# Kernel tuning notes

Measured on AMD Instinct MI355X. Metric: run time of the kernel, lower is better.

The kernel has to match this reference:

```python
import jax, jax.numpy as jnp
from jax import lax
import numpy as np

B, N, NPOINT, NSAMPLE, C = 4, 8192, 2048, 32, 128
RADIUS = 0.2
H1, H2, OUT = 64, 128, 128  # mlp: (3+C)->H1->H2, sas: H2->OUT


def fps(xyz, npoint):
    # furthest point sampling: xyz (B,N,3) -> idx (B,npoint) int32
    b, n, _ = xyz.shape
    init_idx = jnp.zeros((b,), jnp.int32)

    def step(carry, _):
        dist, last = carry
        p = jnp.take_along_axis(xyz, last[:, None, None], axis=1)  # (B,1,3)
        d = jnp.sum((xyz - p) ** 2, axis=-1)                       # (B,N)
        dist = jnp.minimum(dist, d)
        nxt = jnp.argmax(dist, axis=-1).astype(jnp.int32)
        return (dist, nxt), nxt

    (_, _), rest = lax.scan(step, (jnp.full((b, n), 1e10, jnp.float32), init_idx),
                            None, length=npoint - 1)
    return jnp.concatenate([init_idx[None, :], rest], axis=0).T    # (B,npoint)


def ball_query(xyz, new_xyz, radius, nsample):
    # xyz (B,N,3), new_xyz (B,S,3) -> idx (B,S,nsample) int32
    n = xyz.shape[1]
    d2 = jnp.sum((new_xyz[:, :, None, :] - xyz[:, None, :, :]) ** 2, axis=-1)  # (B,S,N)
    ar = jnp.arange(n, dtype=jnp.int32)
    keys = jnp.where(d2 <= radius * radius, ar, n)  # valid -> own index, invalid -> N
    neg_vals, _ = lax.top_k(-keys, nsample)          # smallest nsample keys
    idx = -neg_vals
    first = idx[..., :1]
    return jnp.where(idx >= n, first, idx)           # pad invalid with first valid


def gather_points(pts, idx):
    # pts (B,N,D), idx (B,S,ns) -> (B,S,ns,D)
    b, s, ns = idx.shape
    flat = jnp.take_along_axis(pts, idx.reshape(b, s * ns, 1), axis=1)
    return flat.reshape(b, s, ns, -1)


def setup_inputs() -> dict:
    key = jax.random.key(0)
    ks = jax.random.split(key, 8)
    xyz = jax.random.uniform(ks[0], (B, N, 3), dtype=jnp.float32)
    features = jax.random.normal(ks[1], (B, C, N), dtype=jnp.float32)
    cin = C + 3
    W1 = jax.random.normal(ks[2], (H1, cin), dtype=jnp.float32) / np.sqrt(cin)
    b1 = jnp.zeros((H1,), jnp.float32)
    W2 = jax.random.normal(ks[3], (H2, H1), dtype=jnp.float32) / np.sqrt(H1)
    b2 = jnp.zeros((H2,), jnp.float32)
    Wsa = jax.random.normal(ks[4], (OUT, H2), dtype=jnp.float32) / np.sqrt(H2)
    bsa = jnp.zeros((OUT,), jnp.float32)
    return {"xyz": xyz, "features": features, "W1": W1, "b1": b1,
            "W2": W2, "b2": b2, "Wsa": Wsa, "bsa": bsa}


def reference(xyz, features, W1, b1, W2, b2, Wsa, bsa):
    center_idx = fps(xyz, NPOINT)                                   # (B,S)
    new_xyz = jnp.take_along_axis(xyz, center_idx[:, :, None], axis=1)  # (B,S,3)
    g_idx = ball_query(xyz, new_xyz, RADIUS, NSAMPLE)               # (B,S,ns)
    g_xyz = gather_points(xyz, g_idx) - new_xyz[:, :, None, :]      # (B,S,ns,3) relative coords
    g_feat = gather_points(features.transpose(0, 2, 1), g_idx)      # (B,S,ns,C)
    h = jnp.concatenate([g_xyz, g_feat], axis=-1)                   # (B,S,ns,3+C)
    h = jax.nn.relu(jnp.einsum('bsnc,oc->bsno', h, W1) + b1)        # shared 1x1-conv MLP
    h = jax.nn.relu(jnp.einsum('bsnc,oc->bsno', h, W2) + b2)
    pooled = jnp.max(h, axis=2)                                     # max over nsample -> (B,S,H2)
    out = jnp.einsum('bsc,oc->bso', pooled, Wsa) + bsa              # sas channel mixer
    return new_xyz, out.transpose(0, 2, 1)                          # (B,S,3), (B,OUT,S)
```

## Files before the change

kernel.cpp:

```cpp
#include <hip/hip_runtime.h>
#include <cstdint>
#include <cstddef>

#define NB 4
#define NN 8192
#define NPTS 2048
#define NSAMP 32
#define NC 128
#define CIN 131
#define NH1 64
#define NH2 128
#define NOUTC 128
#define GCELLS 4096

typedef float v2f __attribute__((ext_vector_type(2)));

__device__ __forceinline__ float d2_exact(float ax, float ay, float az,
                                          float bx, float by, float bz) {
  float dx = ax - bx, dy = ay - by, dz = az - bz;
  return __fadd_rn(__fadd_rn(__fmul_rn(dx, dx), __fmul_rn(dy, dy)),
                   __fmul_rn(dz, dz));
}

#if __has_builtin(__builtin_amdgcn_mov_dpp)
template <int CTRL>
__device__ __forceinline__ float dppf(float v) {
  return __int_as_float(
      __builtin_amdgcn_mov_dpp(__float_as_int(v), CTRL, 0xF, 0xF, true));
}
template <int CTRL>
__device__ __forceinline__ int dppi(int v) {
  return __builtin_amdgcn_mov_dpp(v, CTRL, 0xF, 0xF, true);
}
#else
template <int CTRL>
__device__ __forceinline__ float dppf(float v) {
  const int m = (CTRL == 0xB1) ? 1 : (CTRL == 0x4E) ? 2 : (CTRL == 0x141) ? 7 : 15;
  return __shfl_xor(v, m);
}
template <int CTRL>
__device__ __forceinline__ int dppi(int v) {
  const int m = (CTRL == 0xB1) ? 1 : (CTRL == 0x4E) ? 2 : (CTRL == 0x141) ? 7 : 15;
  return __shfl_xor(v, m);
}
#endif

__device__ __forceinline__ void red_pair(float& bv, int& bi, float ov, int oi) {
  bool t = (ov > bv) || (ov == bv && oi < bi);
  bv = t ? ov : bv;
  bi = t ? oi : bi;
}
template <int CTRL>
__device__ __forceinline__ void red5(float& v, int& i, float& x, float& y,
                                     float& z) {
  float ov = dppf<CTRL>(v);
  int oi = dppi<CTRL>(i);
  float ox = dppf<CTRL>(x), oy = dppf<CTRL>(y), oz = dppf<CTRL>(z);
  bool t = (ov > v) || (ov == v && oi < i);
  v = t ? ov : v; i = t ? oi : i;
  x = t ? ox : x; y = t ? oy : y; z = t ? oz : z;
}

__device__ __forceinline__ int spread3(int v) {
  return (v & 1) | ((v & 2) << 2) | ((v & 4) << 4) | ((v & 8) << 6);
}

__global__ __launch_bounds__(1024, 1) void sort_kernel(
    const float* __restrict__ xyz, float* __restrict__ xs,
    float* __restrict__ ys, float* __restrict__ zs, int* __restrict__ io) {
  __shared__ int hist[GCELLS];
  __shared__ int cbase[GCELLS];
  __shared__ int wtot[16];
  __shared__ int woff[16];
  const int b = blockIdx.x;
  const int tid = threadIdx.x;
  const int lane = tid & 63;
  const int wid = tid >> 6;
  const float* xb = xyz + (size_t)b * NN * 3;
  for (int i = tid; i < GCELLS; i += 1024) hist[i] = 0;
  __syncthreads();
  int cell[8];
  float px[8], py[8], pz[8];
#pragma unroll
  for (int k = 0; k < 8; ++k) {
    int j = tid + (k << 10);
    float x = xb[j * 3 + 0], y = xb[j * 3 + 1], z = xb[j * 3 + 2];
    px[k] = x; py[k] = y; pz[k] = z;
    int cx = min(15, max(0, (int)(x * 16.0f)));
    int cy = min(15, max(0, (int)(y * 16.0f)));
    int cz = min(15, max(0, (int)(z * 16.0f)));
    cell[k] = spread3(cx) | (spread3(cy) << 1) | (spread3(cz) << 2);
    atomicAdd(&hist[cell[k]], 1);
  }
  __syncthreads();
  const int i0 = tid * 4;
  int h0 = hist[i0], h1 = hist[i0 + 1], h2 = hist[i0 + 2], h3 = hist[i0 + 3];
  int s4 = h0 + h1 + h2 + h3;
  int v = s4;
#pragma unroll
  for (int d = 1; d < 64; d <<= 1) {
    int o = __shfl_up(v, d);
    if (lane >= d) v += o;
  }
  if (lane == 63) wtot[wid] = v;
  __syncthreads();
  if (tid < 16) {
    int acc = 0;
    for (int w = 0; w < 16; ++w) {
      if (w == tid) woff[tid] = acc;
      acc += wtot[w];
    }
  }
  __syncthreads();
  int eb = woff[wid] + v - s4;
  cbase[i0] = eb;
  cbase[i0 + 1] = eb + h0;
  cbase[i0 + 2] = eb + h0 + h1;
  cbase[i0 + 3] = eb + h0 + h1 + h2;
  __syncthreads();
  for (int i = tid; i < GCELLS; i += 1024) hist[i] = 0;
  __syncthreads();
  const size_t bo = (size_t)b * NN;
#pragma unroll
  for (int k = 0; k < 8; ++k) {
    int pos = cbase[cell[k]] + atomicAdd(&hist[cell[k]], 1);
    xs[bo + pos] = px[k];
    ys[bo + pos] = py[k];
    zs[bo + pos] = zs == nullptr ? 0.f : pz[k];
    io[bo + pos] = tid + (k << 10);
  }
}

__global__ __launch_bounds__(1024, 1) void fps_kernel(
    const float* __restrict__ xyz, const float* __restrict__ xs,
    const float* __restrict__ ys, const float* __restrict__ zs,
    const int* __restrict__ io, float* __restrict__ newxyz) {
#pragma clang fp contract(off)
  const int b = blockIdx.x;
  const int tid = threadIdx.x;
  const int lane = tid & 63;
  const int wid = tid >> 6;
  const size_t bo = (size_t)b * NN;

  float X[8], Y[8], Z[8], D[8];
  int I[8];
  float gcx, gcy, gcz, gr;
  {
    float mx = 0.f, my = 0.f, mz = 0.f;
#pragma unroll
    for (int k = 0; k < 8; ++k) {
      int s = tid * 8 + k;
      X[k] = xs[bo + s];
      Y[k] = ys[bo + s];
      Z[k] = zs[bo + s];
      I[k] = io[bo + s];
      D[k] = 1e30f;
      mx += X[k]; my += Y[k]; mz += Z[k];
    }
    mx *= 0.125f; my *= 0.125f; mz *= 0.125f;
    float r2m = 0.f;
#pragma unroll
    for (int k = 0; k < 8; ++k)
      r2m = fmaxf(r2m, d2_exact(X[k], Y[k], Z[k], mx, my, mz));
    gcx = mx; gcy = my; gcz = mz;
    gr = __fmul_rn(sqrtf(r2m), 1.0001f) + 1e-6f;
  }
  float gv = -1.0f;
  int gidx = 0x3fffffff;
  float bwx = 0.f, bwy = 0.f, bwz = 0.f;
  float T = 3e38f;
  float cv = -1.0f; int ci = 0x3fffffff;
  float ccx = 0.f, ccy = 0.f, ccz = 0.f;

  __shared__ float sv[2][16];
  __shared__ int si[2][16];
  __shared__ float sxx[2][16], syy[2][16], szz[2][16];

  const float* xb = xyz + (size_t)b * NN * 3;
  float cx = xb[0], cy = xb[1], cz = xb[2];
  if (tid == 0) {
    newxyz[(size_t)b * NPTS * 3 + 0] = cx;
    newxyz[(size_t)b * NPTS * 3 + 1] = cy;
    newxyz[(size_t)b * NPTS * 3 + 2] = cz;
  }

  for (int t = 1; t < NPTS; ++t) {
    const int par = t & 1;
    const float d2c = d2_exact(gcx, gcy, gcz, cx, cy, cz);
    const bool dirty = d2c < T;
    if (dirty) {
      float nv = -1.0f; int ni = 0x3fffffff;
      float nx = 0.f, ny = 0.f, nz = 0.f;
#pragma unroll
      for (int k = 0; k < 8; ++k) {
        float d2 = d2_exact(X[k], Y[k], Z[k], cx, cy, cz);
        float nd = fminf(D[k], d2);
        D[k] = nd;
        bool c = (nd > nv) || (nd == nv && I[k] < ni);
        nv = c ? nd : nv; ni = c ? I[k] : ni;
        nx = c ? X[k] : nx; ny = c ? Y[k] : ny; nz = c ? Z[k] : nz;
      }
      gv = nv; gidx = ni; bwx = nx; bwy = ny; bwz = nz;
      float s = __fadd_rn(__fmul_rn(sqrtf(nv), 1.0001f), __fadd_rn(gr, 2e-3f));
      T = __fmul_rn(__fmul_rn(s, s), 1.0001f);
    }
    if (__ballot(dirty) != 0ull) {
      float rv = gv; int ri = gidx;
      red_pair(rv, ri, dppf<0xB1>(rv), dppi<0xB1>(ri));
      red_pair(rv, ri, dppf<0x4E>(rv), dppi<0x4E>(ri));
      red_pair(rv, ri, dppf<0x141>(rv), dppi<0x141>(ri));
      red_pair(rv, ri, dppf<0x140>(rv), dppi<0x140>(ri));
      red_pair(rv, ri, __shfl_xor(rv, 16), __shfl_xor(ri, 16));
      red_pair(rv, ri, __shfl_xor(rv, 32), __shfl_xor(ri, 32));
      unsigned long long m = __ballot(gidx == ri);
      int owner = (int)__builtin_ctzll(m);
      cv = rv; ci = ri;
      ccx = __shfl(bwx, owner);
      ccy = __shfl(bwy, owner);
      ccz = __shfl(bwz, owner);
    }
    if (lane == 0) {
      sv[par][wid] = cv; si[par][wid] = ci;
      sxx[par][wid] = ccx; syy[par][wid] = ccy; szz[par][wid] = ccz;
    }
    __syncthreads();
    const int sl = lane & 15;
    float v = sv[par][sl];
    int i = si[par][sl];
    float xx = sxx[par][sl], yy = syy[par][sl], zz = szz[par][sl];
    red5<0xB1>(v, i, xx, yy, zz);
    red5<0x4E>(v, i, xx, yy, zz);
    red5<0x141>(v, i, xx, yy, zz);
    red5<0x140>(v, i, xx, yy, zz);
    cx = xx; cy = yy; cz = zz;
    if (gidx == i) {
      size_t o = ((size_t)b * NPTS + t) * 3;
      newxyz[o + 0] = xx; newxyz[o + 1] = yy; newxyz[o + 2] = zz;
    }
  }
}

__global__ __launch_bounds__(1024, 1) void fps_nosort_kernel(
    const float* __restrict__ xyz, float* __restrict__ newxyz) {
#pragma clang fp contract(off)
  const int b = blockIdx.x;
  const int tid = threadIdx.x;
  const int lane = tid & 63;
  const int wid = tid >> 6;
  const float* xb = xyz + (size_t)b * NN * 3;
  v2f x2[4], y2[4], z2[4], dd[4];
#pragma unroll
  for (int p = 0; p < 4; ++p) {
    int j0 = tid + ((2 * p) << 10);
    int j1 = tid + ((2 * p + 1) << 10);
    x2[p].x = xb[j0 * 3 + 0]; x2[p].y = xb[j1 * 3 + 0];
    y2[p].x = xb[j0 * 3 + 1]; y2[p].y = xb[j1 * 3 + 1];
    z2[p].x = xb[j0 * 3 + 2]; z2[p].y = xb[j1 * 3 + 2];
    dd[p].x = 1e10f; dd[p].y = 1e10f;
  }
  __shared__ float vbuf[2][16];
  __shared__ int ibuf[2][16];
  __shared__ float cbuf[2][16][3];
  float cx = xb[0], cy = xb[1], cz = xb[2];
  if (tid == 0) {
    newxyz[(size_t)b * NPTS * 3 + 0] = cx;
    newxyz[(size_t)b * NPTS * 3 + 1] = cy;
    newxyz[(size_t)b * NPTS * 3 + 2] = cz;
  }
  for (int t = 1; t < NPTS; ++t) {
    const int par = t & 1;
    float bv = -1.0f; int bi = 0;
    float bwx = 0.f, bwy = 0.f, bwz = 0.f;
#pragma unroll
    for (int p = 0; p < 4; ++p) {
      v2f dx = x2[p] - (v2f){cx, cx};
      v2f dy = y2[p] - (v2f){cy, cy};
      v2f dz = z2[p] - (v2f){cz, cz};
      v2f s = dx * dx + dy * dy + dz * dz;
      v2f nd;
      nd.x = fminf(dd[p].x, s.x);
      nd.y = fminf(dd[p].y, s.y);
      dd[p] = nd;
      { bool c = nd.x > bv;
        bv = c ? nd.x : bv; bi = c ? (tid + ((2 * p) << 10)) : bi;
        bwx = c ? x2[p].x : bwx; bwy = c ? y2[p].x : bwy; bwz = c ? z2[p].x : bwz; }
      { bool c = nd.y > bv;
        bv = c ? nd.y : bv; bi = c ? (tid + ((2 * p + 1) << 10)) : bi;
        bwx = c ? x2[p].y : bwx; bwy = c ? y2[p].y : bwy; bwz = c ? z2[p].y : bwz; }
    }
    red_pair(bv, bi, dppf<0xB1>(bv), dppi<0xB1>(bi));
    red_pair(bv, bi, dppf<0x4E>(bv), dppi<0x4E>(bi));
    red_pair(bv, bi, dppf<0x141>(bv), dppi<0x141>(bi));
    red_pair(bv, bi, dppf<0x140>(bv), dppi<0x140>(bi));
    red_pair(bv, bi, __shfl_xor(bv, 16), __shfl_xor(bi, 16));
    red_pair(bv, bi, __shfl_xor(bv, 32), __shfl_xor(bi, 32));
    if (tid == (bi & 1023)) {
      vbuf[par][wid] = bv; ibuf[par][wid] = bi;
      cbuf[par][wid][0] = bwx; cbuf[par][wid][1] = bwy; cbuf[par][wid][2] = bwz;
    }
    __syncthreads();
    float v2w = vbuf[par][lane & 15];
    int i2w = ibuf[par][lane & 15];
    red_pair(v2w, i2w, dppf<0xB1>(v2w), dppi<0xB1>(i2w));
    red_pair(v2w, i2w, dppf<0x4E>(v2w), dppi<0x4E>(i2w));
    red_pair(v2w, i2w, dppf<0x141>(v2w), dppi<0x141>(i2w));
    red_pair(v2w, i2w, dppf<0x140>(v2w), dppi<0x140>(i2w));
    const int slot = (i2w & 1023) >> 6;
    cx = cbuf[par][slot][0]; cy = cbuf[par][slot][1]; cz = cbuf[par][slot][2];
    if (tid == (i2w & 1023)) {
      size_t o = ((size_t)b * NPTS + t) * 3;
      newxyz[o + 0] = cx; newxyz[o + 1] = cy; newxyz[o + 2] = cz;
    }
  }
}

__global__ __launch_bounds__(256) void ballq_kernel(
    const float* __restrict__ xyz, const float* __restrict__ newxyz,
    int* __restrict__ bidx) {
  const int cid = blockIdx.x * 4 + (threadIdx.x >> 6);
  const int lane = threadIdx.x & 63;
  const int b = cid >> 11;
  const float* xb = xyz + (size_t)b * NN * 3;
  const float cx = newxyz[(size_t)cid * 3 + 0];
  const float cy = newxyz[(size_t)cid * 3 + 1];
  const float cz = newxyz[(size_t)cid * 3 + 2];
  int* ob = bidx + (size_t)cid * NSAMP;
  int total = 0;
  int first = -1;
  for (int c0 = 0; c0 < NN; c0 += 64) {
    int j = c0 + lane;
    float xx = xb[j * 3 + 0], yy = xb[j * 3 + 1], zz = xb[j * 3 + 2];
    float d2 = d2_exact(cx, cy, cz, xx, yy, zz);
    bool in = d2 <= 0.04f;
    unsigned long long m = __ballot(in);
    if (first < 0 && m) first = c0 + __builtin_ctzll(m);
    int pos = total + __popcll(m & ((1ull << lane) - 1ull));
    if (in && pos < NSAMP) ob[pos] = j;
    total += __popcll(m);
    if (total >= NSAMP) break;
  }
  if (total < NSAMP && lane < NSAMP - total) ob[total + lane] = first;
}

__global__ void tw_kernel(const float* __restrict__ W1, const float* __restrict__ W2,
                          const float* __restrict__ Wsa, float* __restrict__ w1t,
                          float* __restrict__ w2t, float* __restrict__ wsat) {
  int i = blockIdx.x * blockDim.x + threadIdx.x;
  if (i < CIN * NH1) w1t[i] = W1[(i % NH1) * CIN + (i / NH1)];
  if (i < NH1 * NH2) w2t[i] = W2[(i % NH2) * NH1 + (i / NH2)];
  if (i < NH2 * NOUTC) wsat[i] = Wsa[(i % NOUTC) * NH2 + (i / NOUTC)];
}

__global__ void tfeat_kernel(const float* __restrict__ feat, float* __restrict__ featT) {
  __shared__ float tile[32][33];
  const int b = blockIdx.z;
  const int n0 = blockIdx.x * 32, c0 = blockIdx.y * 32;
  const int tx = threadIdx.x, ty = threadIdx.y;
#pragma unroll
  for (int r = 0; r < 4; ++r)
    tile[ty + r * 8][tx] = feat[((size_t)b * NC + c0 + ty + r * 8) * NN + n0 + tx];
  __syncthreads();
#pragma unroll
  for (int r = 0; r < 4; ++r)
    featT[((size_t)b * NN + n0 + ty + r * 8) * NC + c0 + tx] = tile[tx][ty + r * 8];
}

#define HS 36
__global__ __launch_bounds__(256) void mlp_kernel(
    const float* __restrict__ xyz, const float* __restrict__ fsrc,
    const float* __restrict__ newxyz, const int* __restrict__ bidx,
    const float* __restrict__ w1t, const float* __restrict__ b1,
    const float* __restrict__ w2t, const float* __restrict__ b2,
    const float* __restrict__ wsat, const float* __restrict__ bsa,
    float* __restrict__ out1, int useT) {
  __shared__ float h[CIN * HS];
  __shared__ float h1[NH1 * HS];
  __shared__ float pl[256];
  __shared__ float pooled[NH2];
  __shared__ int sidx[NSAMP];
  __shared__ float sc[3];
  const int cid = blockIdx.x;
  const int b = cid >> 11;
  const int s = cid & 2047;
  const int tid = threadIdx.x;
  if (tid < NSAMP) sidx[tid] = bidx[(size_t)cid * NSAMP + tid];
  if (tid < 3) sc[tid] = newxyz[(size_t)cid * 3 + tid];
  __syncthreads();
  {
    const int ss = tid >> 3, q = tid & 7;
    const int j = sidx[ss];
    if (useT) {
      const float4* fr = (const float4*)(fsrc + ((size_t)b * NN + j) * NC + q * 16);
#pragma unroll
      for (int u = 0; u < 4; ++u) {
        float4 v = fr[u];
        int c = 3 + q * 16 + u * 4;
        h[(c + 0) * HS + ss] = v.x;
        h[(c + 1) * HS + ss] = v.y;
        h[(c + 2) * HS + ss] = v.z;
        h[(c + 3) * HS + ss] = v.w;
      }
    } else {
      for (int u = 0; u < 16; ++u) {
        int c = q * 16 + u;
        h[(3 + c) * HS + ss] = fsrc[((size_t)b * NC + c) * NN + j];
      }
    }
    if (q == 0) {
      const float* pr = xyz + ((size_t)b * NN + j) * 3;
      h[0 * HS + ss] = pr[0] - sc[0];
      h[1 * HS + ss] = pr[1] - sc[1];
      h[2 * HS + ss] = pr[2] - sc[2];
    }
  }
  __syncthreads();
  {
    const int o = tid & 63, sg = tid >> 6;
    float acc[8];
    const float bb = b1[o];
#pragma unroll
    for (int i = 0; i < 8; ++i) acc[i] = bb;
    const float4* hb = (const float4*)&h[sg * 8];
    for (int k = 0; k < CIN; ++k) {
      float w = w1t[k * NH1 + o];
      float4 a = hb[k * (HS / 4) + 0];
      float4 c = hb[k * (HS / 4) + 1];
      acc[0] = fmaf(w, a.x, acc[0]); acc[1] = fmaf(w, a.y, acc[1]);
      acc[2] = fmaf(w, a.z, acc[2]); acc[3] = fmaf(w, a.w, acc[3]);
      acc[4] = fmaf(w, c.x, acc[4]); acc[5] = fmaf(w, c.y, acc[5]);
      acc[6] = fmaf(w, c.z, acc[6]); acc[7] = fmaf(w, c.w, acc[7]);
    }
#pragma unroll
    for (int i = 0; i < 8; ++i) h1[o * HS + sg * 8 + i] = fmaxf(acc[i], 0.0f);
  }
  __syncthreads();
  {
    const int o = tid & 127, sg = tid >> 7;
    float acc[16];
    const float bb = b2[o];
#pragma unroll
    for (int i = 0; i < 16; ++i) acc[i] = bb;
    const float4* hb = (const float4*)&h1[sg * 16];
    for (int k = 0; k < NH1; ++k) {
      float w = w2t[k * NH2 + o];
#pragma unroll
      for (int u = 0; u < 4; ++u) {
        float4 a = hb[k * (HS / 4) + u];
        acc[u * 4 + 0] = fmaf(w, a.x, acc[u * 4 + 0]);
        acc[u * 4 + 1] = fmaf(w, a.y, acc[u * 4 + 1]);
        acc[u * 4 + 2] = fmaf(w, a.z, acc[u * 4 + 2]);
        acc[u * 4 + 3] = fmaf(w, a.w, acc[u * 4 + 3]);
      }
    }
    float pm = acc[0];
#pragma unroll
    for (int i = 1; i < 16; ++i) pm = fmaxf(pm, acc[i]);
    pl[sg * 128 + o] = pm;
  }
  __syncthreads();
  if (tid < NH2) pooled[tid] = fmaxf(fmaxf(pl[tid], pl[128 + tid]), 0.0f);
  __syncthreads();
  if (tid < NOUTC) {
    float acc = bsa[tid];
    for (int k = 0; k < NH2; ++k) acc = fmaf(pooled[k], wsat[k * NOUTC + tid], acc);
    out1[((size_t)b * NOUTC + tid) * NPTS + s] = acc;
  }
}

extern "C" void kernel_launch(void* const* d_in, const int* in_sizes, int n_in,
                              void* d_out, int out_size, void* d_ws, size_t ws_size,
                              hipStream_t stream) {
  const float* xyz = (const float*)d_in[0];
  const float* feat = (const float*)d_in[1];
  const float* W1 = (const float*)d_in[2];
  const float* b1 = (const float*)d_in[3];
  const float* W2 = (const float*)d_in[4];
  const float* b2 = (const float*)d_in[5];
  const float* Wsa = (const float*)d_in[6];
  const float* bsa = (const float*)d_in[7];
  float* out = (float*)d_out;
  float* newxyz = out;
  float* out1 = out + (size_t)NB * NPTS * 3;

  const size_t sort_f = (size_t)NB * NN * 4;
  const size_t small_f = (size_t)CIN * NH1 + NH1 * NH2 + NH2 * NOUTC +
                         (size_t)NB * NPTS * NSAMP;
  const size_t featT_f = (size_t)NB * NN * NC;

  float* ws = (float*)d_ws;
  bool useSort = ws_size >= (sort_f + small_f) * 4;
  bool useT = ws_size >= (sort_f + small_f + featT_f) * 4;

  float* xs = ws;
  float* ysr = xs + (size_t)NB * NN;
  float* zsr = ysr + (size_t)NB * NN;
  int* iosr = (int*)(zsr + (size_t)NB * NN);
  float* base2 = useSort ? (ws + sort_f) : ws;
  float* w1t = base2;
  float* w2t = w1t + CIN * NH1;
  float* wsat = w2t + NH1 * NH2;
  int* bidx = (int*)(wsat + NH2 * NOUTC);
  float* featT = (float*)(bidx + (size_t)NB * NPTS * NSAMP);

  tw_kernel<<<64, 256, 0, stream>>>(W1, W2, Wsa, w1t, w2t, wsat);
  if (useT)
    tfeat_kernel<<<dim3(NN / 32, NC / 32, NB), dim3(32, 8), 0, stream>>>(feat, featT);
  if (useSort) {
    sort_kernel<<<NB, 1024, 0, stream>>>(xyz, xs, ysr, zsr, iosr);
    fps_kernel<<<NB, 1024, 0, stream>>>(xyz, xs, ysr, zsr, iosr, newxyz);
  } else {
    fps_nosort_kernel<<<NB, 1024, 0, stream>>>(xyz, newxyz);
  }
  ballq_kernel<<<NB * NPTS / 4, 256, 0, stream>>>(xyz, newxyz, bidx);
  mlp_kernel<<<NB * NPTS, 256, 0, stream>>>(xyz, useT ? featT : feat, newxyz, bidx,
                                            w1t, b1, w2t, b2, wsat, bsa, out1,
                                            (int)useT);
}
```

Baseline: 4.096 ms.

## Pick two FPS centers per round using top-2 reduction and halve block size

```diff
diff --git a/kernel.cpp b/kernel.cpp
--- a/kernel.cpp
+++ b/kernel.cpp
@@ -45,20 +45,48 @@
 }
 #endif
 
+__device__ __forceinline__ bool tgt(float av, int ai, float bv, int bi) {
+  return (av > bv) || (av == bv && ai < bi);
+}
+
 __device__ __forceinline__ void red_pair(float& bv, int& bi, float ov, int oi) {
-  bool t = (ov > bv) || (ov == bv && oi < bi);
+  bool t = tgt(ov, oi, bv, bi);
   bv = t ? ov : bv;
   bi = t ? oi : bi;
 }
+
+__device__ __forceinline__ void mergeTop2_vals(float& v1, int& i1, float& v2,
+                                               int& i2, float b1v, int b1i,
+                                               float b2v, int b2i) {
+  bool c = tgt(b1v, b1i, v1, i1);
+  float w1v = c ? b1v : v1; int w1i = c ? b1i : i1;
+  float ltv = c ? v1 : b1v; int lti = c ? i1 : b1i;
+  float wsv = c ? b2v : v2; int wsi = c ? b2i : i2;
+  bool d = tgt(ltv, lti, wsv, wsi);
+  v1 = w1v; i1 = w1i;
+  v2 = d ? ltv : wsv; i2 = d ? lti : wsi;
+}
+
 template <int CTRL>
-__device__ __forceinline__ void red5(float& v, int& i, float& x, float& y,
-                                     float& z) {
-  float ov = dppf<CTRL>(v);
-  int oi = dppi<CTRL>(i);
-  float ox = dppf<CTRL>(x), oy = dppf<CTRL>(y), oz = dppf<CTRL>(z);
-  bool t = (ov > v) || (ov == v && oi < i);
-  v = t ? ov : v; i = t ? oi : i;
-  x = t ? ox : x; y = t ? oy : y; z = t ? oz : z;
+__device__ __forceinline__ void mergeTop2_dpp(float& v1, int& i1, float& x1,
+                                              float& y1, float& z1, float& v2,
+                                              int& i2, float& x2, float& y2,
+                                              float& z2) {
+  float b1v = dppf<CTRL>(v1); int b1i = dppi<CTRL>(i1);
+  float b1x = dppf<CTRL>(x1), b1y = dppf<CTRL>(y1), b1z = dppf<CTRL>(z1);
+  float b2v = dppf<CTRL>(v2); int b2i = dppi<CTRL>(i2);
+  float b2x = dppf<CTRL>(x2), b2y = dppf<CTRL>(y2), b2z = dppf<CTRL>(z2);
+  bool c = tgt(b1v, b1i, v1, i1);
+  float w1v = c ? b1v : v1; int w1i = c ? b1i : i1;
+  float w1x = c ? b1x : x1, w1y = c ? b1y : y1, w1z = c ? b1z : z1;
+  float ltv = c ? v1 : b1v; int lti = c ? i1 : b1i;
+  float ltx = c ? x1 : b1x, lty = c ? y1 : b1y, ltz = c ? z1 : b1z;
+  float wsv = c ? b2v : v2; int wsi = c ? b2i : i2;
+  float wsx = c ? b2x : x2, wsy = c ? b2y : y2, wsz = c ? b2z : z2;
+  bool d = tgt(ltv, lti, wsv, wsi);
+  v1 = w1v; i1 = w1i; x1 = w1x; y1 = w1y; z1 = w1z;
+  v2 = d ? ltv : wsv; i2 = d ? lti : wsi;
+  x2 = d ? ltx : wsx; y2 = d ? lty : wsy; z2 = d ? ltz : wsz;
 }
 
 __device__ __forceinline__ int spread3(int v) {
@@ -126,12 +154,12 @@
     int pos = cbase[cell[k]] + atomicAdd(&hist[cell[k]], 1);
     xs[bo + pos] = px[k];
     ys[bo + pos] = py[k];
-    zs[bo + pos] = zs == nullptr ? 0.f : pz[k];
+    zs[bo + pos] = pz[k];
     io[bo + pos] = tid + (k << 10);
   }
 }
 
-__global__ __launch_bounds__(1024, 1) void fps_kernel(
+__global__ __launch_bounds__(512, 1) void fps_kernel(
     const float* __restrict__ xyz, const float* __restrict__ xs,
     const float* __restrict__ ys, const float* __restrict__ zs,
     const int* __restrict__ io, float* __restrict__ newxyz) {
@@ -142,14 +170,14 @@
   const int wid = tid >> 6;
   const size_t bo = (size_t)b * NN;
 
-  float X[8], Y[8], Z[8], D[8];
-  int I[8];
+  float X[16], Y[16], Z[16], D[16];
+  int I[16];
   float gcx, gcy, gcz, gr;
   {
     float mx = 0.f, my = 0.f, mz = 0.f;
 #pragma unroll
-    for (int k = 0; k < 8; ++k) {
-      int s = tid * 8 + k;
+    for (int k = 0; k < 16; ++k) {
+      int s = tid * 16 + k;
       X[k] = xs[bo + s];
       Y[k] = ys[bo + s];
       Z[k] = zs[bo + s];
@@ -157,86 +185,155 @@
       D[k] = 1e30f;
       mx += X[k]; my += Y[k]; mz += Z[k];
     }
-    mx *= 0.125f; my *= 0.125f; mz *= 0.125f;
+    mx *= 0.0625f; my *= 0.0625f; mz *= 0.0625f;
     float r2m = 0.f;
 #pragma unroll
-    for (int k = 0; k < 8; ++k)
+    for (int k = 0; k < 16; ++k)
       r2m = fmaxf(r2m, d2_exact(X[k], Y[k], Z[k], mx, my, mz));
     gcx = mx; gcy = my; gcz = mz;
     gr = __fmul_rn(sqrtf(r2m), 1.0001f) + 1e-6f;
   }
-  float gv = -1.0f;
-  int gidx = 0x3fffffff;
-  float bwx = 0.f, bwy = 0.f, bwz = 0.f;
+  float e1v = -1.f, e2v = -1.f;
+  int e1i = 0x7fffffff, e2i = 0x7fffffff;
+  float e1x = 0.f, e1y = 0.f, e1z = 0.f, e2x = 0.f, e2y = 0.f, e2z = 0.f;
   float T = 3e38f;
-  float cv = -1.0f; int ci = 0x3fffffff;
-  float ccx = 0.f, ccy = 0.f, ccz = 0.f;
-
-  __shared__ float sv[2][16];
-  __shared__ int si[2][16];
-  __shared__ float sxx[2][16], syy[2][16], szz[2][16];
+  float r1v = -1.f, r2v = -1.f;
+  int r1i = 0x7fffffff, r2i = 0x7fffffff;
+
+  __shared__ float ebuf[2][8][2][8];
 
   const float* xb = xyz + (size_t)b * NN * 3;
-  float cx = xb[0], cy = xb[1], cz = xb[2];
+  float p1x = xb[0], p1y = xb[1], p1z = xb[2];
+  float p2x = p1x, p2y = p1y, p2z = p1z;
+  int npop = 1;
   if (tid == 0) {
-    newxyz[(size_t)b * NPTS * 3 + 0] = cx;
-    newxyz[(size_t)b * NPTS * 3 + 1] = cy;
-    newxyz[(size_t)b * NPTS * 3 + 2] = cz;
-  }
-
-  for (int t = 1; t < NPTS; ++t) {
-    const int par = t & 1;
-    const float d2c = d2_exact(gcx, gcy, gcz, cx, cy, cz);
-    const bool dirty = d2c < T;
-    if (dirty) {
-      float nv = -1.0f; int ni = 0x3fffffff;
-      float nx = 0.f, ny = 0.f, nz = 0.f;
-#pragma unroll
-      for (int k = 0; k < 8; ++k) {
-        float d2 = d2_exact(X[k], Y[k], Z[k], cx, cy, cz);
-        float nd = fminf(D[k], d2);
-        D[k] = nd;
-        bool c = (nd > nv) || (nd == nv && I[k] < ni);
-        nv = c ? nd : nv; ni = c ? I[k] : ni;
-        nx = c ? X[k] : nx; ny = c ? Y[k] : ny; nz = c ? Z[k] : nz;
-      }
-      gv = nv; gidx = ni; bwx = nx; bwy = ny; bwz = nz;
-      float s = __fadd_rn(__fmul_rn(sqrtf(nv), 1.0001f), __fadd_rn(gr, 2e-3f));
+    newxyz[(size_t)b * NPTS * 3 + 0] = p1x;
+    newxyz[(size_t)b * NPTS * 3 + 1] = p1y;
+    newxyz[(size_t)b * NPTS * 3 + 2] = p1z;
+  }
+
+  int t = 1;
+  int rnd = 0;
+  while (t < NPTS) {
+    const int par = rnd & 1;
+    float da = d2_exact(gcx, gcy, gcz, p1x, p1y, p1z);
+    bool dirty = da < T;
+    if (npop == 2) {
+      float db = d2_exact(gcx, gcy, gcz, p2x, p2y, p2z);
+      dirty = dirty || (db < T);
+    }
+    if (__ballot(dirty) != 0ull) {
+      float n1v = -1.f, n2v = -1.f;
+      int n1i = 0x7fffffff, n2i = 0x7fffffff;
+      float n1x = 0.f, n1y = 0.f, n1z = 0.f, n2x = 0.f, n2y = 0.f, n2z = 0.f;
+      if (npop == 2) {
+#pragma unroll
+        for (int k = 0; k < 16; ++k) {
+          float d1 = d2_exact(X[k], Y[k], Z[k], p1x, p1y, p1z);
+          float d2 = d2_exact(X[k], Y[k], Z[k], p2x, p2y, p2z);
+          float nd = fminf(fminf(D[k], d1), d2);
+          D[k] = nd;
+          bool g1 = tgt(nd, I[k], n1v, n1i);
+          bool g2 = tgt(nd, I[k], n2v, n2i);
+          float t2v = g1 ? n1v : (g2 ? nd : n2v);
+          int t2i = g1 ? n1i : (g2 ? I[k] : n2i);
+          float t2x = g1 ? n1x : (g2 ? X[k] : n2x);
+          float t2y = g1 ? n1y : (g2 ? Y[k] : n2y);
+          float t2z = g1 ? n1z : (g2 ? Z[k] : n2z);
+          n1v = g1 ? nd : n1v; n1i = g1 ? I[k] : n1i;
+          n1x = g1 ? X[k] : n1x; n1y = g1 ? Y[k] : n1y; n1z = g1 ? Z[k] : n1z;
+          n2v = t2v; n2i = t2i; n2x = t2x; n2y = t2y; n2z = t2z;
+        }
+      } else {
+#pragma unroll
+        for (int k = 0; k < 16; ++k) {
+          float d1 = d2_exact(X[k], Y[k], Z[k], p1x, p1y, p1z);
+          float nd = fminf(D[k], d1);
+          D[k] = nd;
+          bool g1 = tgt(nd, I[k], n1v, n1i);
+          bool g2 = tgt(nd, I[k], n2v, n2i);
+          float t2v = g1 ? n1v : (g2 ? nd : n2v);
+          int t2i = g1 ? n1i : (g2 ? I[k] : n2i);
+          float t2x = g1 ? n1x : (g2 ? X[k] : n2x);
+          float t2y = g1 ? n1y : (g2 ? Y[k] : n2y);
+          float t2z = g1 ? n1z : (g2 ? Z[k] : n2z);
+          n1v = g1 ? nd : n1v; n1i = g1 ? I[k] : n1i;
+          n1x = g1 ? X[k] : n1x; n1y = g1 ? Y[k] : n1y; n1z = g1 ? Z[k] : n1z;
+          n2v = t2v; n2i = t2i; n2x = t2x; n2y = t2y; n2z = t2z;
+        }
+      }
+      e1v = n1v; e1i = n1i; e1x = n1x; e1y = n1y; e1z = n1z;
+      e2v = n2v; e2i = n2i; e2x = n2x; e2y = n2y; e2z = n2z;
+      float s = __fadd_rn(__fmul_rn(sqrtf(e1v), 1.0001f),
+                          __fadd_rn(gr, 2e-3f));
       T = __fmul_rn(__fmul_rn(s, s), 1.0001f);
-    }
-    if (__ballot(dirty) != 0ull) {
-      float rv = gv; int ri = gidx;
-      red_pair(rv, ri, dppf<0xB1>(rv), dppi<0xB1>(ri));
-      red_pair(rv, ri, dppf<0x4E>(rv), dppi<0x4E>(ri));
-      red_pair(rv, ri, dppf<0x141>(rv), dppi<0x141>(ri));
-      red_pair(rv, ri, dppf<0x140>(rv), dppi<0x140>(ri));
-      red_pair(rv, ri, __shfl_xor(rv, 16), __shfl_xor(ri, 16));
-      red_pair(rv, ri, __shfl_xor(rv, 32), __shfl_xor(ri, 32));
-      unsigned long long m = __ballot(gidx == ri);
-      int owner = (int)__builtin_ctzll(m);
-      cv = rv; ci = ri;
-      ccx = __shfl(bwx, owner);
-      ccy = __shfl(bwy, owner);
-      ccz = __shfl(bwz, owner);
-    }
-    if (lane == 0) {
-      sv[par][wid] = cv; si[par][wid] = ci;
-      sxx[par][wid] = ccx; syy[par][wid] = ccy; szz[par][wid] = ccz;
+      float a1v = e1v, a2v = e2v;
+      int a1i = e1i, a2i = e2i;
+      mergeTop2_vals(a1v, a1i, a2v, a2i, dppf<0xB1>(a1v), dppi<0xB1>(a1i),
+                     dppf<0xB1>(a2v), dppi<0xB1>(a2i));
+      mergeTop2_vals(a1v, a1i, a2v, a2i, dppf<0x4E>(a1v), dppi<0x4E>(a1i),
+                     dppf<0x4E>(a2v), dppi<0x4E>(a2i));
+      mergeTop2_vals(a1v, a1i, a2v, a2i, dppf<0x141>(a1v), dppi<0x141>(a1i),
+                     dppf<0x141>(a2v), dppi<0x141>(a2i));
+      mergeTop2_vals(a1v, a1i, a2v, a2i, dppf<0x140>(a1v), dppi<0x140>(a1i),
+                     dppf<0x140>(a2v), dppi<0x140>(a2i));
+      mergeTop2_vals(a1v, a1i, a2v, a2i, __shfl_xor(a1v, 16),
+                     __shfl_xor(a1i, 16), __shfl_xor(a2v, 16),
+                     __shfl_xor(a2i, 16));
+      mergeTop2_vals(a1v, a1i, a2v, a2i, __shfl_xor(a1v, 32),
+                     __shfl_xor(a1i, 32), __shfl_xor(a2v, 32),
+                     __shfl_xor(a2i, 32));
+      r1v = a1v; r1i = a1i; r2v = a2v; r2i = a2i;
+    }
+    {
+      bool o1a = (e1i == r1i), o1b = (e2i == r1i);
+      if (o1a || o1b) {
+        ebuf[par][wid][0][2] = o1a ? e1x : e2x;
+        ebuf[par][wid][0][3] = o1a ? e1y : e2y;
+        ebuf[par][wid][0][4] = o1a ? e1z : e2z;
+      }
+      bool o2a = (e1i == r2i), o2b = (e2i == r2i);
+      if (o2a || o2b) {
+        ebuf[par][wid][1][2] = o2a ? e1x : e2x;
+        ebuf[par][wid][1][3] = o2a ? e1y : e2y;
+        ebuf[par][wid][1][4] = o2a ? e1z : e2z;
+      }
+      if (lane == 0) {
+        ebuf[par][wid][0][0] = r1v;
+        ebuf[par][wid][0][1] = __int_as_float(r1i);
+        ebuf[par][wid][1][0] = r2v;
+        ebuf[par][wid][1][1] = __int_as_float(r2i);
+      }
     }
     __syncthreads();
-    const int sl = lane & 15;
-    float v = sv[par][sl];
-    int i = si[par][sl];
-    float xx = sxx[par][sl], yy = syy[par][sl], zz = szz[par][sl];
-    red5<0xB1>(v, i, xx, yy, zz);
-    red5<0x4E>(v, i, xx, yy, zz);
-    red5<0x141>(v, i, xx, yy, zz);
-    red5<0x140>(v, i, xx, yy, zz);
-    cx = xx; cy = yy; cz = zz;
-    if (gidx == i) {
+    const int w = lane & 7, e = (lane >> 3) & 1;
+    const float* ep = &ebuf[par][w][e][0];
+    float m1v = ep[0];
+    int m1i = __float_as_int(ep[1]);
+    float m1x = ep[2], m1y = ep[3], m1z = ep[4];
+    float m2v = -1.f; int m2i = 0x7fffffff;
+    float m2x = 0.f, m2y = 0.f, m2z = 0.f;
+    mergeTop2_dpp<0xB1>(m1v, m1i, m1x, m1y, m1z, m2v, m2i, m2x, m2y, m2z);
+    mergeTop2_dpp<0x4E>(m1v, m1i, m1x, m1y, m1z, m2v, m2i, m2x, m2y, m2z);
+    mergeTop2_dpp<0x141>(m1v, m1i, m1x, m1y, m1z, m2v, m2i, m2x, m2y, m2z);
+    mergeTop2_dpp<0x140>(m1v, m1i, m1x, m1y, m1z, m2v, m2i, m2x, m2y, m2z);
+    bool pop2 = false;
+    if (t + 1 < NPTS) {
+      float q = d2_exact(m2x, m2y, m2z, m1x, m1y, m1z);
+      pop2 = (q >= m2v);
+    }
+    if (tid == 0) {
       size_t o = ((size_t)b * NPTS + t) * 3;
-      newxyz[o + 0] = xx; newxyz[o + 1] = yy; newxyz[o + 2] = zz;
-    }
+      newxyz[o + 0] = m1x; newxyz[o + 1] = m1y; newxyz[o + 2] = m1z;
+      if (pop2) {
+        newxyz[o + 3] = m2x; newxyz[o + 4] = m2y; newxyz[o + 5] = m2z;
+      }
+    }
+    p1x = m1x; p1y = m1y; p1z = m1z;
+    p2x = m2x; p2y = m2y; p2z = m2z;
+    npop = pop2 ? 2 : 1;
+    t += npop;
+    ++rnd;
   }
 }
 
@@ -507,7 +604,7 @@
     tfeat_kernel<<<dim3(NN / 32, NC / 32, NB), dim3(32, 8), 0, stream>>>(feat, featT);
   if (useSort) {
     sort_kernel<<<NB, 1024, 0, stream>>>(xyz, xs, ysr, zsr, iosr);
-    fps_kernel<<<NB, 1024, 0, stream>>>(xyz, xs, ysr, zsr, iosr, newxyz);
+    fps_kernel<<<NB, 512, 0, stream>>>(xyz, xs, ysr, zsr, iosr, newxyz);
   } else {
     fps_nosort_kernel<<<NB, 1024, 0, stream>>>(xyz, newxyz);
   }
```

Result: faster. 3.906 ms (-4.6%).
